# Performance work log

Hardware: AMD Instinct MI355X
Metric: run time of the kernel (lower is better)

The kernel has to match this reference:

```python
import jax, jax.numpy as jnp
import numpy as np

EPS_BN = 1e-5
EPS_NORM = 1e-12
TOP_K = 512


def _conv(x, w):
    # NCHW conv, stride 1, SAME padding (ultralytics Conv autopad)
    return jax.lax.conv_general_dilated(x, w, (1, 1), 'SAME',
                                        dimension_numbers=('NCHW', 'OIHW', 'NCHW'))


def _bn(x, g, b, m, v):
    # inference-mode BatchNorm2d
    inv = jax.lax.rsqrt(v + EPS_BN)
    return (x - m[None, :, None, None]) * (g * inv)[None, :, None, None] + b[None, :, None, None]


def _descriptor(feat, p):
    (w_dr, g_dr, b_dr, m_dr, v_dr,
     w_d1, g_d1, b_d1, m_d1, v_d1,
     g_e, b_e, m_e, v_e,
     w_d2, g_d2, b_d2, m_d2, v_d2) = p
    # dim_reduce: Conv(channel, channel//2, 1) = conv+BN+SiLU
    x = jax.nn.silu(_bn(_conv(feat, w_dr), g_dr, b_dr, m_dr, v_dr))
    # descriptor: Conv(c/2, c/2, 3) + BN + ReLU + Conv(c/2, c/4, 1)
    x = jax.nn.silu(_bn(_conv(x, w_d1), g_d1, b_d1, m_d1, v_d1))
    x = jax.nn.relu(_bn(x, g_e, b_e, m_e, v_e))
    x = jax.nn.silu(_bn(_conv(x, w_d2), g_d2, b_d2, m_d2, v_d2))
    return x


def _keypoints(desc):
    b, c, h, w = desc.shape
    resp = jnp.sqrt(jnp.sum(desc * desc, axis=1)).reshape(b, h * w)  # L2 norm over channels
    _, idx = jax.lax.top_k(resp, TOP_K)                              # [b, K]
    y = (idx // w).astype(desc.dtype) / (h - 1) * 2 - 1
    x = (idx % w).astype(desc.dtype) / (w - 1) * 2 - 1
    return jnp.stack([x, y], axis=-1), idx                           # [b,K,2], [b,K]


def _forward(rgb_feat, ir_feat, params):
    rgb_desc = _descriptor(rgb_feat, params)
    ir_desc = _descriptor(ir_feat, params)

    kp1, idx1 = _keypoints(rgb_desc)
    kp2, idx2 = _keypoints(ir_desc)

    b, c, h, w = rgb_desc.shape
    hw = h * w
    d1 = rgb_desc.reshape(b, c, hw)
    d2 = ir_desc.reshape(b, c, hw)
    d1 = d1 / jnp.maximum(jnp.linalg.norm(d1, axis=1, keepdims=True), EPS_NORM)
    d2 = d2 / jnp.maximum(jnp.linalg.norm(d2, axis=1, keepdims=True), EPS_NORM)
    corr = jnp.einsum('bcn,bcm->bnm', d1, d2)     # [b, hw, hw]
    soft = jax.nn.softmax(corr, axis=-1)

    # scalar matching weight per keypoint pair (gather at keypoint locations)
    bidx = jnp.arange(b)[:, None]
    wts = soft[bidx, idx1, idx2]                  # [b, K]

    # vectorized DLT: A rows, two per point, weighted
    x1, y1 = kp1[..., 0], kp1[..., 1]
    x2, y2 = kp2[..., 0], kp2[..., 1]
    one = jnp.ones_like(x1)
    zer = jnp.zeros_like(x1)
    r1 = jnp.stack([x1, y1, one, zer, zer, zer, -x2 * x1, -x2 * y1, -x2], axis=-1)
    r2 = jnp.stack([zer, zer, zer, x1, y1, one, -y2 * x1, -y2 * y1, -y2], axis=-1)
    A = jnp.stack([r1, r2], axis=2) * wts[:, :, None, None]   # [b,K,2,9]
    A = A.reshape(b, 2 * TOP_K, 9)

    _, _, Vh = jnp.linalg.svd(A, full_matrices=False)          # Vh: [b,9,9]
    # torch.svd returns V; original takes V[-1] == last COLUMN of jax Vh
    H = Vh[:, :, -1].reshape(b, 3, 3)
    return H, rgb_desc, ir_desc


def setup_inputs() -> dict:
    key = jax.random.key(0)
    ks = jax.random.split(key, 8)
    B, C, Hh, Ww = 2, 256, 64, 64
    c2, c4 = C // 2, C // 4
    f32 = jnp.float32

    def bn_params(c):
        return (jnp.ones((c,), f32), jnp.zeros((c,), f32),
                jnp.zeros((c,), f32), jnp.ones((c,), f32))

    g_dr, b_dr, m_dr, v_dr = bn_params(c2)
    g_d1, b_d1, m_d1, v_d1 = bn_params(c2)
    g_e, b_e, m_e, v_e = bn_params(c2)
    g_d2, b_d2, m_d2, v_d2 = bn_params(c4)

    return {
        'rgb_feat': jax.random.normal(ks[0], (B, C, Hh, Ww), f32),
        'ir_feat': jax.random.normal(ks[1], (B, C, Hh, Ww), f32),
        'w_dr': jax.random.normal(ks[2], (c2, C, 1, 1), f32) * 0.05,
        'g_dr': g_dr, 'b_dr': b_dr, 'm_dr': m_dr, 'v_dr': v_dr,
        'w_d1': jax.random.normal(ks[3], (c2, c2, 3, 3), f32) * 0.05,
        'g_d1': g_d1, 'b_d1': b_d1, 'm_d1': m_d1, 'v_d1': v_d1,
        'g_e': g_e, 'b_e': b_e, 'm_e': m_e, 'v_e': v_e,
        'w_d2': jax.random.normal(ks[4], (c4, c2, 1, 1), f32) * 0.05,
        'g_d2': g_d2, 'b_d2': b_d2, 'm_d2': m_d2, 'v_d2': v_d2,
    }


def reference(rgb_feat, ir_feat,
              w_dr, g_dr, b_dr, m_dr, v_dr,
              w_d1, g_d1, b_d1, m_d1, v_d1,
              g_e, b_e, m_e, v_e,
              w_d2, g_d2, b_d2, m_d2, v_d2):
    params = (w_dr, g_dr, b_dr, m_dr, v_dr,
              w_d1, g_d1, b_d1, m_d1, v_d1,
              g_e, b_e, m_e, v_e,
              w_d2, g_d2, b_d2, m_d2, v_d2)
    return _forward(rgb_feat, ir_feat, params)
```

## Files before the change

### kernel.cpp

```cpp
#include <hip/hip_runtime.h>
#include <math.h>


#define HW4 4096
#define NIMG 4

#define OFF_X1   0L
#define OFF_X2   (OFF_X1 + 4L*128*4096)
#define OFF_RESP (OFF_X2 + 4L*128*4096)
#define OFF_INVN (OFF_RESP + 4L*4096)
#define OFF_TOPI (OFF_INVN + 4L*4096)
#define OFF_WTS  (OFF_TOPI + 4L*512)
#define OFF_A    (OFF_WTS + 2L*512)
#define OFF_QN   OFF_X1
#define OFF_PART (OFF_X1 + 65536L)

#define NSPLIT 16

__device__ __forceinline__ float silu_f(float y) { return y / (1.f + expf(-y)); }

__global__ __launch_bounds__(256) void fm_conv1(
    const float* __restrict__ rgb, const float* __restrict__ ir,
    const float* __restrict__ w, const float* __restrict__ g,
    const float* __restrict__ bb, const float* __restrict__ mm,
    const float* __restrict__ vv, float* __restrict__ x1) {
  __shared__ float wl[256*8];
  int bid = blockIdx.x;
  int pblk = bid & 3, ocg = (bid >> 2) & 15, img = bid >> 6;
  int oc0 = ocg * 8;
  int tid = threadIdx.x;
  const float* src = (img < 2) ? (rgb + (long)img*256*HW4) : (ir + (long)(img-2)*256*HW4);
  for (int i = tid; i < 2048; i += 256) {
    int o = i & 7, ic = i >> 3;
    wl[i] = w[(oc0 + o)*256 + ic];
  }
  __syncthreads();
  int p0 = pblk*1024 + tid*4;
  float acc[8][4];
  #pragma unroll
  for (int o = 0; o < 8; ++o)
    #pragma unroll
    for (int j = 0; j < 4; ++j) acc[o][j] = 0.f;
  #pragma unroll 4
  for (int ic = 0; ic < 256; ++ic) {
    float4 v = *(const float4*)(src + (long)ic*HW4 + p0);
    float4 wa = *(const float4*)&wl[ic*8];
    float4 wb = *(const float4*)&wl[ic*8 + 4];
    acc[0][0] = fmaf(wa.x, v.x, acc[0][0]); acc[0][1] = fmaf(wa.x, v.y, acc[0][1]);
    acc[0][2] = fmaf(wa.x, v.z, acc[0][2]); acc[0][3] = fmaf(wa.x, v.w, acc[0][3]);
    acc[1][0] = fmaf(wa.y, v.x, acc[1][0]); acc[1][1] = fmaf(wa.y, v.y, acc[1][1]);
    acc[1][2] = fmaf(wa.y, v.z, acc[1][2]); acc[1][3] = fmaf(wa.y, v.w, acc[1][3]);
    acc[2][0] = fmaf(wa.z, v.x, acc[2][0]); acc[2][1] = fmaf(wa.z, v.y, acc[2][1]);
    acc[2][2] = fmaf(wa.z, v.z, acc[2][2]); acc[2][3] = fmaf(wa.z, v.w, acc[2][3]);
    acc[3][0] = fmaf(wa.w, v.x, acc[3][0]); acc[3][1] = fmaf(wa.w, v.y, acc[3][1]);
    acc[3][2] = fmaf(wa.w, v.z, acc[3][2]); acc[3][3] = fmaf(wa.w, v.w, acc[3][3]);
    acc[4][0] = fmaf(wb.x, v.x, acc[4][0]); acc[4][1] = fmaf(wb.x, v.y, acc[4][1]);
    acc[4][2] = fmaf(wb.x, v.z, acc[4][2]); acc[4][3] = fmaf(wb.x, v.w, acc[4][3]);
    acc[5][0] = fmaf(wb.y, v.x, acc[5][0]); acc[5][1] = fmaf(wb.y, v.y, acc[5][1]);
    acc[5][2] = fmaf(wb.y, v.z, acc[5][2]); acc[5][3] = fmaf(wb.y, v.w, acc[5][3]);
    acc[6][0] = fmaf(wb.z, v.x, acc[6][0]); acc[6][1] = fmaf(wb.z, v.y, acc[6][1]);
    acc[6][2] = fmaf(wb.z, v.z, acc[6][2]); acc[6][3] = fmaf(wb.z, v.w, acc[6][3]);
    acc[7][0] = fmaf(wb.w, v.x, acc[7][0]); acc[7][1] = fmaf(wb.w, v.y, acc[7][1]);
    acc[7][2] = fmaf(wb.w, v.z, acc[7][2]); acc[7][3] = fmaf(wb.w, v.w, acc[7][3]);
  }
  #pragma unroll
  for (int o = 0; o < 8; ++o) {
    int oc = oc0 + o;
    float inv = 1.f / sqrtf(vv[oc] + 1e-5f);
    float sc = g[oc]*inv, sh = bb[oc] - mm[oc]*sc;
    float4 r;
    r.x = silu_f(acc[o][0]*sc + sh);
    r.y = silu_f(acc[o][1]*sc + sh);
    r.z = silu_f(acc[o][2]*sc + sh);
    r.w = silu_f(acc[o][3]*sc + sh);
    r.x = silu_f((acc[o][0] - mm[oc])*sc + bb[oc]);
    r.y = silu_f((acc[o][1] - mm[oc])*sc + bb[oc]);
    r.z = silu_f((acc[o][2] - mm[oc])*sc + bb[oc]);
    r.w = silu_f((acc[o][3] - mm[oc])*sc + bb[oc]);
    *(float4*)(x1 + ((long)img*128 + oc)*HW4 + p0) = r;
  }
}

#define C3_TW 72
#define C3_TR 18
__global__ __launch_bounds__(256) void fm_conv3(
    const float* __restrict__ x1, const float* __restrict__ w,
    const float* __restrict__ g1, const float* __restrict__ b1,
    const float* __restrict__ m1, const float* __restrict__ v1,
    const float* __restrict__ ge, const float* __restrict__ be,
    const float* __restrict__ me, const float* __restrict__ ve,
    float* __restrict__ x2) {
  __shared__ float t[2][4][C3_TR*C3_TW];
  __shared__ float wl[2][4][9][8];
  int bid = blockIdx.x;
  int rt = bid & 3, ocg = (bid >> 2) & 15, img = bid >> 6;
  int oc0 = ocg * 8;
  int y0 = rt * 16;
  int tid = threadIdx.x;
  int ly = tid >> 4;
  int lx = tid & 15;
  int x0 = lx * 4;
  const float* xim = x1 + (long)img*128*HW4;

  int gbase[5][4];
  int lofs[5];
  #pragma unroll
  for (int t5 = 0; t5 < 5; ++t5) {
    int i = tid + 256*t5;
    if (i < 1224) {
      int q = i / 306, r = i - q*306;
      int row = r / 17, seg = r - row*17;
      int gy = y0 + row - 1;
      lofs[t5] = q*(C3_TR*C3_TW) + row*C3_TW + 4 + seg*4;
      #pragma unroll
      for (int e = 0; e < 4; ++e) {
        int x = seg*4 + e - 1;
        gbase[t5][e] = (gy >= 0 && gy < 64 && x >= 0 && x < 64)
                       ? (q*HW4 + gy*64 + x) : -1;
      }
    } else {
      lofs[t5] = -1;
      #pragma unroll
      for (int e = 0; e < 4; ++e) gbase[t5][e] = -1;
    }
  }
  int wg0 = -1, wl0 = 0, wg1 = -1, wl1 = 0;
  {
// ... 283 lines not shown
      part[idx] = m[r];
      part[idx + 1] = s[r];
    }
  }
}

__global__ __launch_bounds__(256) void fm_comb(
    const float* __restrict__ out, const float* __restrict__ invn,
    const int* __restrict__ topidx, const float* __restrict__ qn,
    const float* __restrict__ part, float* __restrict__ wts) {
  int tid = threadIdx.x;
  int kp = blockIdx.x*4 + (tid >> 6);
  int lane = tid & 63;
  int b = kp >> 9, k = kp & 511;
  int col = topidx[(2 + b)*512 + k];
  const float* d2 = out + 18 + (long)(2 + b)*262144;
  float dot = qn[(long)kp*64 + lane] * d2[lane*HW4 + col];
  #pragma unroll
  for (int off = 1; off < 64; off <<= 1) dot += __shfl_xor(dot, off);
  if (lane == 0) {
    const float* pp = part + (long)kp*NSPLIT*2;
    float M = -INFINITY;
    #pragma unroll
    for (int i = 0; i < NSPLIT; ++i) M = fmaxf(M, pp[2*i]);
    float S = 0.f;
    #pragma unroll
    for (int i = 0; i < NSPLIT; ++i) S += pp[2*i + 1]*expf(pp[2*i] - M);
    float v = dot * invn[(long)(2 + b)*HW4 + col];
    wts[b*512 + k] = expf(v - M)/S;
  }
}

__global__ __launch_bounds__(256) void fm_build(
    const int* __restrict__ topidx, const float* __restrict__ wts,
    float* __restrict__ A) {
  int t = blockIdx.x*256 + threadIdx.x;
  if (t >= 1024) return;
  int b = t >> 9, k = t & 511;
  int i1 = topidx[b*512 + k], i2 = topidx[(2 + b)*512 + k];
  float w = wts[b*512 + k];
  float x1 = (float)(i1 & 63) / 63.f * 2.f - 1.f;
  float y1 = (float)(i1 >> 6) / 63.f * 2.f - 1.f;
  float x2 = (float)(i2 & 63) / 63.f * 2.f - 1.f;
  float y2 = (float)(i2 >> 6) / 63.f * 2.f - 1.f;
  float* r = A + ((long)b*1024 + 2*k)*9;
  r[0] = x1*w;  r[1] = y1*w;  r[2] = w;
  r[3] = 0.f;   r[4] = 0.f;   r[5] = 0.f;
  r[6] = (-x2*x1)*w; r[7] = (-x2*y1)*w; r[8] = (-x2)*w;
  r[9]  = 0.f;  r[10] = 0.f;  r[11] = 0.f;
  r[12] = x1*w; r[13] = y1*w; r[14] = w;
  r[15] = (-y2*x1)*w; r[16] = (-y2*y1)*w; r[17] = (-y2)*w;
}

__device__ void lap_slartg(float f, float g, float* cs, float* sn, float* r) {
  if (g == 0.f) { *cs = 1.f; *sn = 0.f; *r = f; }
  else if (f == 0.f) { *cs = 0.f; *sn = copysignf(1.f, g); *r = fabsf(g); }
  else {
    float d = sqrtf(f*f + g*g);
    *cs = fabsf(f) / d;
    *r = copysignf(d, f);
    *sn = g / (*r);
  }
}

__device__ void lap_slas2(float f, float g, float h, float* ssmin, float* ssmax) {
  float fa = fabsf(f), ga = fabsf(g), ha = fabsf(h);
  float fhmn = fminf(fa, ha), fhmx = fmaxf(fa, ha);
  if (fhmn == 0.f) {
    *ssmin = 0.f;
    if (fhmx == 0.f) *ssmax = ga;
    else {
      float mx = fmaxf(fhmx, ga), mn = fminf(fhmx, ga);
      float q = mn / mx;
      *ssmax = mx * sqrtf(1.f + q*q);
    }
  } else {
    if (ga < fhmx) {
      float as_ = 1.f + fhmn/fhmx;
      float at_ = (fhmx - fhmn)/fhmx;
      float au = ga/fhmx; au = au*au;
      float c = 2.f / (sqrtf(as_*as_ + au) + sqrtf(at_*at_ + au));
      *ssmin = fhmn*c;
      *ssmax = fhmx/c;
    } else {
      float au = fhmx/ga;
      if (au == 0.f) { *ssmin = (fhmn*fhmx)/ga; *ssmax = ga; }
      else {
        float as_ = 1.f + fhmn/fhmx;
        float at_ = (fhmx - fhmn)/fhmx;
        float t1 = as_*au, t2 = at_*au;
        float c = 1.f / (sqrtf(1.f + t1*t1) + sqrtf(1.f + t2*t2));
        float smn = (fhmn*c)*au;
        *ssmin = smn + smn;
        *ssmax = ga/(c + c);
      }
    }
  }
}

__device__ void lap_slasv2(float f, float g, float h, float* ssmin, float* ssmax,
                           float* snr, float* csr, float* snl, float* csl) {
  const float epsv = 5.9604645e-08f;
  float ft = f, fa = fabsf(f), ht = h, ha = fabsf(h);
  int pmax = 1;
  bool swap_ = (ha > fa);
  if (swap_) { pmax = 3; float tmp = ft; ft = ht; ht = tmp; tmp = fa; fa = ha; ha = tmp; }
  float gt = g, ga = fabsf(gt);
  float clt = 0.f, crt = 0.f, slt = 0.f, srt = 0.f;
  if (ga == 0.f) { *ssmin = ha; *ssmax = fa; clt = 1.f; crt = 1.f; slt = 0.f; srt = 0.f; }
  else {
    bool gasmal = true;
    if (ga > fa) {
      pmax = 2;
      if ((fa/ga) < epsv) {
        gasmal = false;
        *ssmax = ga;
        if (ha > 1.f) *ssmin = fa/(ga/ha); else *ssmin = (fa/ga)*ha;
        clt = 1.f; slt = ht/gt; srt = 1.f; crt = ft/gt;
      }
    }
    if (gasmal) {
      float d = fa - ha, l;
      if (d == fa) l = 1.f; else l = d/fa;
      float m_ = gt/ft;
      float t = 2.f - l;
      float mm2 = m_*m_, tt = t*t;
      float s = sqrtf(tt + mm2);
      float r_ = (l == 0.f) ? fabsf(m_) : sqrtf(l*l + mm2);
      float a = 0.5f*(s + r_);
      *ssmin = ha/a;
      *ssmax = fa*a;
      if (mm2 == 0.f) {
        if (l == 0.f) t = copysignf(2.f, ft)*copysignf(1.f, gt);
        else t = gt/copysignf(d, ft) + m_/t;
      } else {
        t = (m_/(s + t) + m_/(r_ + l))*(1.f + a);
      }
      float l2 = sqrtf(t*t + 4.f);
      crt = 2.f/l2;
      srt = t/l2;
      clt = (crt + srt*m_)/a;
      slt = (ht/ft)*srt/a;
    }
  }
  if (swap_) { *csl = srt; *snl = crt; *csr = slt; *snr = clt; }
  else { *csl = clt; *snl = slt; *csr = crt; *snr = srt; }
  float tsign = 1.f;
  if (pmax == 1) tsign = copysignf(1.f, *csr)*copysignf(1.f, *csl)*copysignf(1.f, f);
  if (pmax == 2) tsign = copysignf(1.f, *snr)*copysignf(1.f, *csl)*copysignf(1.f, g);
  if (pmax == 3) tsign = copysignf(1.f, *snr)*copysignf(1.f, *snl)*copysignf(1.f, h);
  *ssmax = copysignf(*ssmax, tsign);
  *ssmin = copysignf(*ssmin, tsign*copysignf(1.f, f)*copysignf(1.f, h));
}

__device__ void lap_bdsqr9(float* dd, float* ee, float VT[][9]) {
  const float eps_ = 5.9604645e-08f;
  const float unfl_ = 1.17549435e-38f;
  const float tol_ = 10.f*eps_;
  const int n = 9;
  for (int i = 0; i < 9; ++i) for (int j = 0; j < 9; ++j) VT[i][j] = (i == j) ? 1.f : 0.f;
  float sminoa = fabsf(dd[0]);
  if (sminoa != 0.f) {
    float mu = sminoa;
    for (int i = 1; i < n; ++i) {
      mu = fabsf(dd[i])*(mu/(mu + fabsf(ee[i-1])));
      sminoa = fminf(sminoa, mu);
      if (sminoa == 0.f) break;
    }
  }
  sminoa = sminoa / 3.f;
  float thresh = fmaxf(tol_*sminoa, 486.f*unfl_);
  int m = n, iter = 0, oldll = -1, oldm = -1, idir = 0;
  float sminl = 0.f;
  float rc[8], rs[8];
  int guard = 0;
  while (guard++ < 20000) {
    if (m <= 1) break;
    if (iter > 486) break;
    float smax = fabsf(dd[m-1]);
    int ll = 0; bool split = false;
    for (int lll = 1; lll <= m - 1; ++lll) {
      int l2 = m - lll;
      float abss = fabsf(dd[l2-1]);
      float abse = fabsf(ee[l2-1]);
      if (abse <= thresh) { ll = l2; split = true; break; }
      smax = fmaxf(smax, fmaxf(abss, abse));
    }
    if (split) {
      ee[ll-1] = 0.f;
      if (ll == m - 1) { m = m - 1; continue; }
    } else ll = 0;
    ll = ll + 1;
    if (ll == m - 1) {
      float sigmn, sigmx, sinr, cosr, sinl_, cosl_;
      lap_slasv2(dd[m-2], ee[m-2], dd[m-1], &sigmn, &sigmx, &sinr, &cosr, &sinl_, &cosl_);
      dd[m-2] = sigmx; ee[m-2] = 0.f; dd[m-1] = sigmn;
      for (int j = 0; j < 9; ++j) {
        float xt = VT[m-2][j], yt = VT[m-1][j];
        VT[m-2][j] = cosr*xt + sinr*yt;
        VT[m-1][j] = cosr*yt - sinr*xt;
      }
      m -= 2; continue;
    }
    if (ll > oldm || m < oldll) idir = (fabsf(dd[ll-1]) >= fabsf(dd[m-1])) ? 1 : 2;
    bool conv = false;
    if (idir == 1) {
      if (fabsf(ee[m-2]) <= tol_*fabsf(dd[m-1])) { ee[m-2] = 0.f; continue; }
      float mu = fabsf(dd[ll-1]);
      sminl = mu;
      for (int lll = ll; lll <= m - 1; ++lll) {
        if (fabsf(ee[lll-1]) <= tol_*mu) { ee[lll-1] = 0.f; conv = true; break; }
        mu = fabsf(dd[lll])*(mu/(mu + fabsf(ee[lll-1])));
        sminl = fminf(sminl, mu);
      }
    } else {
      if (fabsf(ee[ll-1]) <= tol_*fabsf(dd[ll-1])) { ee[ll-1] = 0.f; continue; }
      float mu = fabsf(dd[m-1]);
      sminl = mu;
      for (int lll = m - 1; lll >= ll; --lll) {
        if (fabsf(ee[lll-1]) <= tol_*mu) { ee[lll-1] = 0.f; conv = true; break; }
        mu = fabsf(dd[lll-1])*(mu/(mu + fabsf(ee[lll-1])));
        sminl = fminf(sminl, mu);
      }
    }
    if (conv) continue;
    oldll = ll; oldm = m;
    float shift = 0.f, rdum;
    if (!((float)n*tol_*(sminl/smax) <= fmaxf(eps_, 0.01f*tol_))) {
      float sll;
      if (idir == 1) { sll = fabsf(dd[ll-1]); lap_slas2(dd[m-2], ee[m-2], dd[m-1], &shift, &rdum); }
      else           { sll = fabsf(dd[m-1]);  lap_slas2(dd[ll-1], ee[ll-1], dd[ll], &shift, &rdum); }
      if (sll > 0.f) { float q = shift/sll; if (q*q < eps_) shift = 0.f; }
    }
    iter += m - ll;
    if (shift == 0.f) {
      if (idir == 1) {
        float cs = 1.f, oldcs = 1.f, sn = 0.f, oldsn = 0.f, r;
        for (int i = ll; i <= m - 1; ++i) {
          lap_slartg(dd[i-1]*cs, ee[i-1], &cs, &sn, &r);
          if (i > ll) ee[i-2] = oldsn*r;
          float dn;
          lap_slartg(oldcs*r, dd[i]*sn, &oldcs, &oldsn, &dn);
          dd[i-1] = dn;
          rc[i-ll] = cs; rs[i-ll] = sn;
        }
        float h2 = dd[m-1]*cs;
        dd[m-1] = h2*oldcs;
        ee[m-2] = h2*oldsn;
        for (int k2 = 0; k2 <= m - ll - 1; ++k2) {
          int r0 = ll + k2 - 1;
          float c = rc[k2], s = rs[k2];
          for (int j = 0; j < 9; ++j) {
            float t = VT[r0+1][j];
            VT[r0+1][j] = c*t - s*VT[r0][j];
            VT[r0][j]   = s*t + c*VT[r0][j];
          }
        }
        if (fabsf(ee[m-2]) <= thresh) ee[m-2] = 0.f;
      } else {
        float cs = 1.f, oldcs = 1.f, sn = 0.f, oldsn = 0.f, r;
        for (int i = m; i >= ll + 1; --i) {
          lap_slartg(dd[i-1]*cs, ee[i-2], &cs, &sn, &r);
          if (i < m) ee[i-1] = oldsn*r;
          float dn;
          lap_slartg(oldcs*r, dd[i-2]*sn, &oldcs, &oldsn, &dn);
          dd[i-1] = dn;
          rc[i-ll-1] = oldcs; rs[i-ll-1] = -oldsn;
        }
        float h2 = dd[ll-1]*cs;
        dd[ll-1] = h2*oldcs;
        ee[ll-1] = h2*oldsn;
        for (int k2 = m - ll - 1; k2 >= 0; --k2) {
          int r0 = ll + k2 - 1;
          float c = rc[k2], s = rs[k2];
          for (int j = 0; j < 9; ++j) {
            float t = VT[r0+1][j];
            VT[r0+1][j] = c*t - s*VT[r0][j];
            VT[r0][j]   = s*t + c*VT[r0][j];
          }
        }
        if (fabsf(ee[ll-1]) <= thresh) ee[ll-1] = 0.f;
      }
    } else {
      if (idir == 1) {
        float f2 = (fabsf(dd[ll-1]) - shift)*(copysignf(1.f, dd[ll-1]) + shift/dd[ll-1]);
        float g2 = ee[ll-1];
        for (int i = ll; i <= m - 1; ++i) {
          float cr, sr, cl, sl, r;
          lap_slartg(f2, g2, &cr, &sr, &r);
          if (i > ll) ee[i-2] = r;
          f2 = cr*dd[i-1] + sr*ee[i-1];
          ee[i-1] = cr*ee[i-1] - sr*dd[i-1];
          g2 = sr*dd[i];
          dd[i] = cr*dd[i];
          lap_slartg(f2, g2, &cl, &sl, &r);
          dd[i-1] = r;
          f2 = cl*ee[i-1] + sl*dd[i];
          dd[i] = cl*dd[i] - sl*ee[i-1];
          if (i < m - 1) { g2 = sl*ee[i]; ee[i] = cl*ee[i]; }
          rc[i-ll] = cr; rs[i-ll] = sr;
        }
        ee[m-2] = f2;
        for (int k2 = 0; k2 <= m - ll - 1; ++k2) {
          int r0 = ll + k2 - 1;
          float c = rc[k2], s = rs[k2];
          for (int j = 0; j < 9; ++j) {
            float t = VT[r0+1][j];
            VT[r0+1][j] = c*t - s*VT[r0][j];
            VT[r0][j]   = s*t + c*VT[r0][j];
          }
        }
        if (fabsf(ee[m-2]) <= thresh) ee[m-2] = 0.f;
      } else {
        float f2 = (fabsf(dd[m-1]) - shift)*(copysignf(1.f, dd[m-1]) + shift/dd[m-1]);
        float g2 = ee[m-2];
        for (int i = m; i >= ll + 1; --i) {
          float cr, sr, cl, sl, r;
          lap_slartg(f2, g2, &cr, &sr, &r);
          if (i < m) ee[i-1] = r;
          f2 = cr*dd[i-1] + sr*ee[i-2];
          ee[i-2] = cr*ee[i-2] - sr*dd[i-1];
          g2 = sr*dd[i-2];
          dd[i-2] = cr*dd[i-2];
          lap_slartg(f2, g2, &cl, &sl, &r);
          dd[i-1] = r;
          f2 = cl*ee[i-2] + sl*dd[i-2];
          dd[i-2] = cl*dd[i-2] - sl*ee[i-2];
          if (i > ll + 1) { g2 = sl*ee[i-3]; ee[i-3] = cl*ee[i-3]; }
          rc[i-ll-1] = cl; rs[i-ll-1] = -sl;
        }
        ee[ll-1] = f2;
        if (fabsf(ee[ll-1]) <= thresh) ee[ll-1] = 0.f;
        for (int k2 = m - ll - 1; k2 >= 0; --k2) {
          int r0 = ll + k2 - 1;
          float c = rc[k2], s = rs[k2];
          for (int j = 0; j < 9; ++j) {
            float t = VT[r0+1][j];
            VT[r0+1][j] = c*t - s*VT[r0][j];
            VT[r0][j]   = s*t + c*VT[r0][j];
          }
        }
      }
    }
  }
  for (int i = 0; i < n; ++i) {
    if (dd[i] < 0.f) {
      dd[i] = -dd[i];
      for (int j = 0; j < 9; ++j) VT[i][j] = -VT[i][j];
    }
  }
  for (int i = 1; i <= n - 1; ++i) {
    int isub = 1; float smin2 = dd[0];
    for (int j = 2; j <= n + 1 - i; ++j)
      if (dd[j-1] <= smin2) { isub = j; smin2 = dd[j-1]; }
    int tgt = n + 1 - i;
    if (isub != tgt) {
      dd[isub-1] = dd[tgt-1]; dd[tgt-1] = smin2;
      for (int j = 0; j < 9; ++j) {
        float t = VT[isub-1][j]; VT[isub-1][j] = VT[tgt-1][j]; VT[tgt-1][j] = t;
      }
    }
  }
}

__global__ __launch_bounds__(256) void fm_svd(
    const float* __restrict__ Aglob, float* __restrict__ outH) {
  __shared__ float As[1024*9];
  __shared__ float red[256];
  __shared__ float bc[4];
  __shared__ float Rm[9][9], VT[9][9], PT[9][9];
  __shared__ float dd[9], ee[9], taup[9];
  int b = blockIdx.x, tid = threadIdx.x;
  const float* Ab = Aglob + (long)b*1024*9;
  for (int i = tid; i < 9216; i += 256) As[i] = Ab[i];
  __syncthreads();
  for (int k = 0; k < 9; ++k) {
    float ps = 0.f;
    for (int r = k + 1 + tid; r < 1024; r += 256) { float x = As[r*9 + k]; ps = fmaf(x, x, ps); }
    red[tid] = ps; __syncthreads();
    for (int off = 128; off > 0; off >>= 1) {
      if (tid < off) red[tid] += red[tid + off];
      __syncthreads();
    }
    if (tid == 0) {
      float ssq = red[0];
      float alpha = As[k*9 + k];
      float tau = 0.f, sc = 0.f, beta = alpha;
      if (ssq != 0.f) {
        beta = -copysignf(sqrtf(alpha*alpha + ssq), alpha);
        tau = (beta - alpha)/beta;
        sc = 1.f/(alpha - beta);
      }
      bc[0] = tau; bc[1] = sc; bc[2] = beta;
    }
    __syncthreads();
    float tau = bc[0], sc = bc[1];
    if (tau != 0.f) {
      for (int r = k + 1 + tid; r < 1024; r += 256) As[r*9 + k] *= sc;
    }
    __syncthreads();
    if (tau != 0.f) {
      for (int j = k + 1; j < 9; ++j) {
        float pd = 0.f;
        for (int r = k + 1 + tid; r < 1024; r += 256) pd = fmaf(As[r*9 + k], As[r*9 + j], pd);
        red[tid] = pd; __syncthreads();
        for (int off = 128; off > 0; off >>= 1) {
          if (tid < off) red[tid] += red[tid + off];
          __syncthreads();
        }
        float s = (red[0] + As[k*9 + j]) * tau;
        if (tid == 0) As[k*9 + j] -= s;
        for (int r = k + 1 + tid; r < 1024; r += 256) As[r*9 + j] -= s*As[r*9 + k];
        __syncthreads();
      }
    }
    if (tid == 0) As[k*9 + k] = bc[2];
    __syncthreads();
  }
  if (tid == 0) {
    for (int i = 0; i < 9; ++i)
      for (int j = 0; j < 9; ++j)
        Rm[i][j] = (j >= i) ? As[i*9 + j] : 0.f;
    for (int i = 0; i < 9; ++i) {
      float alpha = Rm[i][i];
      float ssq = 0.f;
      for (int r = i + 1; r < 9; ++r) ssq += Rm[r][i]*Rm[r][i];
      float tauq = 0.f, beta = alpha;
      if (ssq != 0.f) {
        beta = -copysignf(sqrtf(alpha*alpha + ssq), alpha);
        tauq = (beta - alpha)/beta;
        float sc = 1.f/(alpha - beta);
        for (int r = i + 1; r < 9; ++r) Rm[r][i] *= sc;
      }
      dd[i] = beta;
      if (tauq != 0.f) {
        for (int j = i + 1; j < 9; ++j) {
          float s = Rm[i][j];
          for (int r = i + 1; r < 9; ++r) s += Rm[r][i]*Rm[r][j];
          s *= tauq;
          Rm[i][j] -= s;
          for (int r = i + 1; r < 9; ++r) Rm[r][j] -= s*Rm[r][i];
        }
      }
      if (i < 8) {
        float alpha2 = Rm[i][i+1];
        float ssq2 = 0.f;
        for (int c = i + 2; c < 9; ++c) ssq2 += Rm[i][c]*Rm[i][c];
        float tp = 0.f, beta2 = alpha2;
        if (ssq2 != 0.f) {
          beta2 = -copysignf(sqrtf(alpha2*alpha2 + ssq2), alpha2);
          tp = (beta2 - alpha2)/beta2;
          float sc = 1.f/(alpha2 - beta2);
          for (int c = i + 2; c < 9; ++c) Rm[i][c] *= sc;
        }
        ee[i] = beta2;
        taup[i] = tp;
        if (tp != 0.f) {
          for (int r = i + 1; r < 9; ++r) {
            float s = Rm[r][i+1];
            for (int c = i + 2; c < 9; ++c) s += Rm[i][c]*Rm[r][c];
            s *= tp;
            Rm[r][i+1] -= s;
            for (int c = i + 2; c < 9; ++c) Rm[r][c] -= s*Rm[i][c];
          }
        }
      }
    }
    for (int i = 0; i < 9; ++i) for (int j = 0; j < 9; ++j) PT[i][j] = (i == j) ? 1.f : 0.f;
    for (int i = 0; i < 8; ++i) {
      float tp = taup[i];
      if (tp == 0.f) continue;
      for (int j = 0; j < 9; ++j) {
        float s = PT[i+1][j];
        for (int r = i + 2; r < 9; ++r) s += Rm[i][r]*PT[r][j];
        s *= tp;
        PT[i+1][j] -= s;
        for (int r = i + 2; r < 9; ++r) PT[r][j] -= s*Rm[i][r];
      }
    }
    lap_bdsqr9(dd, ee, VT);
    for (int i = 0; i < 9; ++i) {
      float s = 0.f;
      for (int k2 = 0; k2 < 9; ++k2) s += VT[i][k2]*PT[k2][8];
      outH[b*9 + i] = s;
    }
  }
}

extern "C" void kernel_launch(void* const* d_in, const int* in_sizes, int n_in,
                              void* d_out, int out_size, void* d_ws, size_t ws_size,
                              hipStream_t stream) {
  const float* rgb  = (const float*)d_in[0];
  const float* ir   = (const float*)d_in[1];
  const float* w_dr = (const float*)d_in[2];
  const float* g_dr = (const float*)d_in[3];
  const float* b_dr = (const float*)d_in[4];
  const float* m_dr = (const float*)d_in[5];
  const float* v_dr = (const float*)d_in[6];
  const float* w_d1 = (const float*)d_in[7];
  const float* g_d1 = (const float*)d_in[8];
  const float* b_d1 = (const float*)d_in[9];
  const float* m_d1 = (const float*)d_in[10];
  const float* v_d1 = (const float*)d_in[11];
  const float* g_e  = (const float*)d_in[12];
  const float* b_e  = (const float*)d_in[13];
  const float* m_e  = (const float*)d_in[14];
  const float* v_e  = (const float*)d_in[15];
  const float* w_d2 = (const float*)d_in[16];
  const float* g_d2 = (const float*)d_in[17];
  const float* b_d2 = (const float*)d_in[18];
  const float* m_d2 = (const float*)d_in[19];
  const float* v_d2 = (const float*)d_in[20];

  float* out = (float*)d_out;
  float* ws  = (float*)d_ws;
  float* x1   = ws + OFF_X1;
  float* x2   = ws + OFF_X2;
  float* resp = ws + OFF_RESP;
  float* invn = ws + OFF_INVN;
  int*   topi = (int*)(ws + OFF_TOPI);
  float* wts  = ws + OFF_WTS;
  float* Amat = ws + OFF_A;
  float* qn   = ws + OFF_QN;
  float* part = ws + OFF_PART;

  fm_conv1<<<256, 256, 0, stream>>>(rgb, ir, w_dr, g_dr, b_dr, m_dr, v_dr, x1);
  fm_conv3<<<256, 256, 0, stream>>>(x1, w_d1, g_d1, b_d1, m_d1, v_d1,
                                    g_e, b_e, m_e, v_e, x2);
  fm_conv2<<<256, 256, 0, stream>>>(x2, w_d2, g_d2, b_d2, m_d2, v_d2, out);
  fm_resp<<<(NIMG*HW4 + 255)/256, 256, 0, stream>>>(out, resp, invn);
  fm_sort<<<NIMG, 1024, 0, stream>>>(resp, topi);
  fm_qgather<<<256, 256, 0, stream>>>(out, invn, topi, qn);
  fm_corr<<<dim3(NSPLIT, 16, 2), 256, 0, stream>>>(out, invn, qn, part);
  fm_comb<<<256, 256, 0, stream>>>(out, invn, topi, qn, part, wts);
  fm_build<<<4, 256, 0, stream>>>(topi, wts, Amat);
  fm_svd<<<2, 256, 0, stream>>>(Amat, out);
}
// ... 1 lines not shown
```

Before: 443.5 us.

## Move SVD small-matrix stage into registers with wavefront shuffles and batched reflector updates

Restructures the fm_svd kernel. The Householder QR of the 1024x9 system now replaces 256-thread LDS tree reductions with wave shuffle reductions, and batches all column dot products per reflector so one reduction and sync pass covers them. The 9x9 bidiagonalization and bdsqr iterations now run in registers: each of the first 9 lanes tracks one column of VT instead of a single thread rotating a shared 9x9 matrix. Only column 8 of PT is built. Fully unrolled predicated loops add register pressure and extra instructions. The iteration guard is also reduced, and a dead BN epilogue duplicate is removed from conv1.

```diff
diff --git a/kernel.cpp b/kernel.cpp
--- a/kernel.cpp
+++ b/kernel.cpp
@@ -67,12 +67,8 @@
   for (int o = 0; o < 8; ++o) {
     int oc = oc0 + o;
     float inv = 1.f / sqrtf(vv[oc] + 1e-5f);
-    float sc = g[oc]*inv, sh = bb[oc] - mm[oc]*sc;
+    float sc = g[oc]*inv;
     float4 r;
-    r.x = silu_f(acc[o][0]*sc + sh);
-    r.y = silu_f(acc[o][1]*sc + sh);
-    r.z = silu_f(acc[o][2]*sc + sh);
-    r.w = silu_f(acc[o][3]*sc + sh);
     r.x = silu_f((acc[o][0] - mm[oc])*sc + bb[oc]);
     r.y = silu_f((acc[o][1] - mm[oc])*sc + bb[oc]);
     r.z = silu_f((acc[o][2] - mm[oc])*sc + bb[oc]);
@@ -462,7 +458,7 @@
   r[15] = (-y2*x1)*w; r[16] = (-y2*y1)*w; r[17] = (-y2)*w;
 }
 
-__device__ void lap_slartg(float f, float g, float* cs, float* sn, float* r) {
+__device__ __forceinline__ void lap_slartg(float f, float g, float* cs, float* sn, float* r) {
   if (g == 0.f) { *cs = 1.f; *sn = 0.f; *r = f; }
   else if (f == 0.f) { *cs = 0.f; *sn = copysignf(1.f, g); *r = fabsf(g); }
   else {
@@ -473,7 +469,7 @@
   }
 }
 
-__device__ void lap_slas2(float f, float g, float h, float* ssmin, float* ssmax) {
+__device__ __forceinline__ void lap_slas2(float f, float g, float h, float* ssmin, float* ssmax) {
   float fa = fabsf(f), ga = fabsf(g), ha = fabsf(h);
   float fhmn = fminf(fa, ha), fhmx = fmaxf(fa, ha);
   if (fhmn == 0.f) {
@@ -508,7 +504,7 @@
   }
 }
 
-__device__ void lap_slasv2(float f, float g, float h, float* ssmin, float* ssmax,
+__device__ __forceinline__ void lap_slasv2(float f, float g, float h, float* ssmin, float* ssmax,
                            float* snr, float* csr, float* snl, float* csl) {
   const float epsv = 5.9604645e-08f;
   float ft = f, fa = fabsf(f), ht = h, ha = fabsf(h);
@@ -563,212 +559,220 @@
   *ssmin = copysignf(*ssmin, tsign*copysignf(1.f, f)*copysignf(1.f, h));
 }
 
-__device__ void lap_bdsqr9(float* dd, float* ee, float VT[][9]) {
+__device__ __forceinline__ float get9(const float (&a)[9], int idx) {
+  float v = a[0];
+#pragma unroll
+  for (int i = 1; i < 9; ++i) if (idx == i) v = a[i];
+  return v;
+}
+__device__ __forceinline__ void set9(float (&a)[9], int idx, float val) {
+#pragma unroll
+  for (int i = 0; i < 9; ++i) if (idx == i) a[i] = val;
+}
+
+__device__ __forceinline__ void bdsqr9_reg(float (&dd)[9], float (&ee)[9], float (&vt)[9]) {
   const float eps_ = 5.9604645e-08f;
   const float unfl_ = 1.17549435e-38f;
   const float tol_ = 10.f*eps_;
-  const int n = 9;
-  for (int i = 0; i < 9; ++i) for (int j = 0; j < 9; ++j) VT[i][j] = (i == j) ? 1.f : 0.f;
   float sminoa = fabsf(dd[0]);
   if (sminoa != 0.f) {
     float mu = sminoa;
-    for (int i = 1; i < n; ++i) {
-      mu = fabsf(dd[i])*(mu/(mu + fabsf(ee[i-1])));
-      sminoa = fminf(sminoa, mu);
-      if (sminoa == 0.f) break;
+    bool z = false;
+#pragma unroll
+    for (int i = 1; i < 9; ++i) {
+      if (!z) {
+        mu = fabsf(dd[i])*(mu/(mu + fabsf(ee[i-1])));
+        sminoa = fminf(sminoa, mu);
+        if (sminoa == 0.f) z = true;
+      }
     }
   }
   sminoa = sminoa / 3.f;
   float thresh = fmaxf(tol_*sminoa, 486.f*unfl_);
-  int m = n, iter = 0, oldll = -1, oldm = -1, idir = 0;
+  int m = 9, iter = 0, oldll = -1, oldm = -1, idir = 0;
   float sminl = 0.f;
-  float rc[8], rs[8];
   int guard = 0;
-  while (guard++ < 20000) {
+  while (guard++ < 2000) {
     if (m <= 1) break;
     if (iter > 486) break;
-    float smax = fabsf(dd[m-1]);
+    float smax = fabsf(get9(dd, m-1));
     int ll = 0; bool split = false;
-    for (int lll = 1; lll <= m - 1; ++lll) {
-      int l2 = m - lll;
-      float abss = fabsf(dd[l2-1]);
-      float abse = fabsf(ee[l2-1]);
-      if (abse <= thresh) { ll = l2; split = true; break; }
-      smax = fmaxf(smax, fmaxf(abss, abse));
+#pragma unroll
+    for (int l2 = 8; l2 >= 1; --l2) {
+      if (l2 <= m - 1 && !split) {
+        float abss = fabsf(dd[l2-1]);
+        float abse = fabsf(ee[l2-1]);
+        if (abse <= thresh) { ll = l2; split = true; }
+        else smax = fmaxf(smax, fmaxf(abss, abse));
+      }
     }
     if (split) {
-      ee[ll-1] = 0.f;
+      set9(ee, ll-1, 0.f);
       if (ll == m - 1) { m = m - 1; continue; }
     } else ll = 0;
     ll = ll + 1;
     if (ll == m - 1) {
+      float d1 = get9(dd, m-2), e1 = get9(ee, m-2), d2v = get9(dd, m-1);
       float sigmn, sigmx, sinr, cosr, sinl_, cosl_;
-      lap_slasv2(dd[m-2], ee[m-2], dd[m-1], &sigmn, &sigmx, &sinr, &cosr, &sinl_, &cosl_);
-      dd[m-2] = sigmx; ee[m-2] = 0.f; dd[m-1] = sigmn;
-      for (int j = 0; j < 9; ++j) {
-        float xt = VT[m-2][j], yt = VT[m-1][j];
-        VT[m-2][j] = cosr*xt + sinr*yt;
-        VT[m-1][j] = cosr*yt - sinr*xt;
-      }
+      lap_slasv2(d1, e1, d2v, &sigmn, &sigmx, &sinr, &cosr, &sinl_, &cosl_);
+      set9(dd, m-2, sigmx); set9(ee, m-2, 0.f); set9(dd, m-1, sigmn);
+      float xt = get9(vt, m-2), yt = get9(vt, m-1);
+      set9(vt, m-2, cosr*xt + sinr*yt);
+      set9(vt, m-1, cosr*yt - sinr*xt);
       m -= 2; continue;
     }
-    if (ll > oldm || m < oldll) idir = (fabsf(dd[ll-1]) >= fabsf(dd[m-1])) ? 1 : 2;
+    if (ll > oldm || m < oldll)
+      idir = (fabsf(get9(dd, ll-1)) >= fabsf(get9(dd, m-1))) ? 1 : 2;
     bool conv = false;
     if (idir == 1) {
-      if (fabsf(ee[m-2]) <= tol_*fabsf(dd[m-1])) { ee[m-2] = 0.f; continue; }
-      float mu = fabsf(dd[ll-1]);
+      if (fabsf(get9(ee, m-2)) <= tol_*fabsf(get9(dd, m-1))) { set9(ee, m-2, 0.f); continue; }
+      float mu = fabsf(get9(dd, ll-1));
       sminl = mu;
-      for (int lll = ll; lll <= m - 1; ++lll) {
-        if (fabsf(ee[lll-1]) <= tol_*mu) { ee[lll-1] = 0.f; conv = true; break; }
-        mu = fabsf(dd[lll])*(mu/(mu + fabsf(ee[lll-1])));
-        sminl = fminf(sminl, mu);
+#pragma unroll
+      for (int lll = 1; lll <= 8; ++lll) {
+        if (lll >= ll && lll <= m - 1 && !conv) {
+          if (fabsf(ee[lll-1]) <= tol_*mu) { ee[lll-1] = 0.f; conv = true; }
+          else {
+            mu = fabsf(dd[lll])*(mu/(mu + fabsf(ee[lll-1])));
+            sminl = fminf(sminl, mu);
+          }
+        }
       }
     } else {
-      if (fabsf(ee[ll-1]) <= tol_*fabsf(dd[ll-1])) { ee[ll-1] = 0.f; continue; }
-      float mu = fabsf(dd[m-1]);
+      if (fabsf(get9(ee, ll-1)) <= tol_*fabsf(get9(dd, ll-1))) { set9(ee, ll-1, 0.f); continue; }
+      float mu = fabsf(get9(dd, m-1));
       sminl = mu;
-      for (int lll = m - 1; lll >= ll; --lll) {
-        if (fabsf(ee[lll-1]) <= tol_*mu) { ee[lll-1] = 0.f; conv = true; break; }
-        mu = fabsf(dd[lll-1])*(mu/(mu + fabsf(ee[lll-1])));
-        sminl = fminf(sminl, mu);
+#pragma unroll
+      for (int lll = 8; lll >= 1; --lll) {
+        if (lll <= m - 1 && lll >= ll && !conv) {
+          if (fabsf(ee[lll-1]) <= tol_*mu) { ee[lll-1] = 0.f; conv = true; }
+          else {
+            mu = fabsf(dd[lll-1])*(mu/(mu + fabsf(ee[lll-1])));
+            sminl = fminf(sminl, mu);
+          }
+        }
       }
     }
     if (conv) continue;
     oldll = ll; oldm = m;
     float shift = 0.f, rdum;
-    if (!((float)n*tol_*(sminl/smax) <= fmaxf(eps_, 0.01f*tol_))) {
+    if (!(9.f*tol_*(sminl/smax) <= fmaxf(eps_, 0.01f*tol_))) {
       float sll;
-      if (idir == 1) { sll = fabsf(dd[ll-1]); lap_slas2(dd[m-2], ee[m-2], dd[m-1], &shift, &rdum); }
-      else           { sll = fabsf(dd[m-1]);  lap_slas2(dd[ll-1], ee[ll-1], dd[ll], &shift, &rdum); }
+      if (idir == 1) { sll = fabsf(get9(dd, ll-1)); lap_slas2(get9(dd, m-2), get9(ee, m-2), get9(dd, m-1), &shift, &rdum); }
+      else           { sll = fabsf(get9(dd, m-1));  lap_slas2(get9(dd, ll-1), get9(ee, ll-1), get9(dd, ll), &shift, &rdum); }
       if (sll > 0.f) { float q = shift/sll; if (q*q < eps_) shift = 0.f; }
     }
     iter += m - ll;
     if (shift == 0.f) {
       if (idir == 1) {
         float cs = 1.f, oldcs = 1.f, sn = 0.f, oldsn = 0.f, r;
-        for (int i = ll; i <= m - 1; ++i) {
-          lap_slartg(dd[i-1]*cs, ee[i-1], &cs, &sn, &r);
-          if (i > ll) ee[i-2] = oldsn*r;
-          float dn;
-          lap_slartg(oldcs*r, dd[i]*sn, &oldcs, &oldsn, &dn);
-          dd[i-1] = dn;
-          rc[i-ll] = cs; rs[i-ll] = sn;
-        }
-        float h2 = dd[m-1]*cs;
-        dd[m-1] = h2*oldcs;
-        ee[m-2] = h2*oldsn;
-        for (int k2 = 0; k2 <= m - ll - 1; ++k2) {
-          int r0 = ll + k2 - 1;
-          float c = rc[k2], s = rs[k2];
-          for (int j = 0; j < 9; ++j) {
-            float t = VT[r0+1][j];
-            VT[r0+1][j] = c*t - s*VT[r0][j];
-            VT[r0][j]   = s*t + c*VT[r0][j];
+#pragma unroll
+        for (int i = 1; i <= 8; ++i) {
+          if (i >= ll && i <= m - 1) {
+            lap_slartg(dd[i-1]*cs, ee[i-1], &cs, &sn, &r);
+            if (i >= 2 && i > ll) ee[i-2] = oldsn*r;
+            float dn;
+            lap_slartg(oldcs*r, dd[i]*sn, &oldcs, &oldsn, &dn);
+            dd[i-1] = dn;
+            float t = vt[i]; vt[i] = cs*t - sn*vt[i-1]; vt[i-1] = sn*t + cs*vt[i-1];
           }
         }
-        if (fabsf(ee[m-2]) <= thresh) ee[m-2] = 0.f;
+        float h2 = get9(dd, m-1)*cs;
+        set9(dd, m-1, h2*oldcs);
+        set9(ee, m-2, h2*oldsn);
+        if (fabsf(get9(ee, m-2)) <= thresh) set9(ee, m-2, 0.f);
       } else {
         float cs = 1.f, oldcs = 1.f, sn = 0.f, oldsn = 0.f, r;
-        for (int i = m; i >= ll + 1; --i) {
-          lap_slartg(dd[i-1]*cs, ee[i-2], &cs, &sn, &r);
-          if (i < m) ee[i-1] = oldsn*r;
-          float dn;
-          lap_slartg(oldcs*r, dd[i-2]*sn, &oldcs, &oldsn, &dn);
-          dd[i-1] = dn;
-          rc[i-ll-1] = oldcs; rs[i-ll-1] = -oldsn;
-        }
-        float h2 = dd[ll-1]*cs;
-        dd[ll-1] = h2*oldcs;
-        ee[ll-1] = h2*oldsn;
-        for (int k2 = m - ll - 1; k2 >= 0; --k2) {
-          int r0 = ll + k2 - 1;
-          float c = rc[k2], s = rs[k2];
-          for (int j = 0; j < 9; ++j) {
-            float t = VT[r0+1][j];
-            VT[r0+1][j] = c*t - s*VT[r0][j];
-            VT[r0][j]   = s*t + c*VT[r0][j];
+#pragma unroll
+        for (int i = 9; i >= 2; --i) {
+          if (i <= m && i >= ll + 1) {
+            lap_slartg(dd[i-1]*cs, ee[i-2], &cs, &sn, &r);
+            if (i < m) ee[i-1] = oldsn*r;
+            float dn;
+            lap_slartg(oldcs*r, dd[i-2]*sn, &oldcs, &oldsn, &dn);
+            dd[i-1] = dn;
+            float c2 = oldcs, s2 = -oldsn;
+            float t = vt[i-1]; vt[i-1] = c2*t - s2*vt[i-2]; vt[i-2] = s2*t + c2*vt[i-2];
           }
         }
-        if (fabsf(ee[ll-1]) <= thresh) ee[ll-1] = 0.f;
+        float h2 = get9(dd, ll-1)*cs;
+        set9(dd, ll-1, h2*oldcs);
+        set9(ee, ll-1, h2*oldsn);
+        if (fabsf(get9(ee, ll-1)) <= thresh) set9(ee, ll-1, 0.f);
       }
     } else {
       if (idir == 1) {
-        float f2 = (fabsf(dd[ll-1]) - shift)*(copysignf(1.f, dd[ll-1]) + shift/dd[ll-1]);
-        float g2 = ee[ll-1];
-        for (int i = ll; i <= m - 1; ++i) {
-          float cr, sr, cl, sl, r;
-          lap_slartg(f2, g2, &cr, &sr, &r);
-          if (i > ll) ee[i-2] = r;
-          f2 = cr*dd[i-1] + sr*ee[i-1];
-          ee[i-1] = cr*ee[i-1] - sr*dd[i-1];
-          g2 = sr*dd[i];
-          dd[i] = cr*dd[i];
-          lap_slartg(f2, g2, &cl, &sl, &r);
-          dd[i-1] = r;
-          f2 = cl*ee[i-1] + sl*dd[i];
-          dd[i] = cl*dd[i] - sl*ee[i-1];
-          if (i < m - 1) { g2 = sl*ee[i]; ee[i] = cl*ee[i]; }
-          rc[i-ll] = cr; rs[i-ll] = sr;
-        }
-        ee[m-2] = f2;
-        for (int k2 = 0; k2 <= m - ll - 1; ++k2) {
-          int r0 = ll + k2 - 1;
-          float c = rc[k2], s = rs[k2];
-          for (int j = 0; j < 9; ++j) {
-            float t = VT[r0+1][j];
-            VT[r0+1][j] = c*t - s*VT[r0][j];
-            VT[r0][j]   = s*t + c*VT[r0][j];
+        float d0 = get9(dd, ll-1);
+        float f2 = (fabsf(d0) - shift)*(copysignf(1.f, d0) + shift/d0);
+        float g2 = get9(ee, ll-1);
+#pragma unroll
+        for (int i = 1; i <= 8; ++i) {
+          if (i >= ll && i <= m - 1) {
+            float cr, sr, cl, sl, r;
+            lap_slartg(f2, g2, &cr, &sr, &r);
+            if (i >= 2 && i > ll) ee[i-2] = r;
+            f2 = cr*dd[i-1] + sr*ee[i-1];
+            ee[i-1] = cr*ee[i-1] - sr*dd[i-1];
+            g2 = sr*dd[i];
+            dd[i] = cr*dd[i];
+            lap_slartg(f2, g2, &cl, &sl, &r);
+            dd[i-1] = r;
+            f2 = cl*ee[i-1] + sl*dd[i];
+            dd[i] = cl*dd[i] - sl*ee[i-1];
+            if (i < m - 1) { g2 = sl*ee[i]; ee[i] = cl*ee[i]; }
+            float t = vt[i]; vt[i] = cr*t - sr*vt[i-1]; vt[i-1] = sr*t + cr*vt[i-1];
           }
         }
-        if (fabsf(ee[m-2]) <= thresh) ee[m-2] = 0.f;
+        set9(ee, m-2, f2);
+        if (fabsf(get9(ee, m-2)) <= thresh) set9(ee, m-2, 0.f);
       } else {
-        float f2 = (fabsf(dd[m-1]) - shift)*(copysignf(1.f, dd[m-1]) + shift/dd[m-1]);
-        float g2 = ee[m-2];
-        for (int i = m; i >= ll + 1; --i) {
-          float cr, sr, cl, sl, r;
-          lap_slartg(f2, g2, &cr, &sr, &r);
-          if (i < m) ee[i-1] = r;
-          f2 = cr*dd[i-1] + sr*ee[i-2];
-          ee[i-2] = cr*ee[i-2] - sr*dd[i-1];
-          g2 = sr*dd[i-2];
-          dd[i-2] = cr*dd[i-2];
-          lap_slartg(f2, g2, &cl, &sl, &r);
-          dd[i-1] = r;
-          f2 = cl*ee[i-2] + sl*dd[i-2];
-          dd[i-2] = cl*dd[i-2] - sl*ee[i-2];
-          if (i > ll + 1) { g2 = sl*ee[i-3]; ee[i-3] = cl*ee[i-3]; }
-          rc[i-ll-1] = cl; rs[i-ll-1] = -sl;
-        }
-        ee[ll-1] = f2;
-        if (fabsf(ee[ll-1]) <= thresh) ee[ll-1] = 0.f;
-        for (int k2 = m - ll - 1; k2 >= 0; --k2) {
-          int r0 = ll + k2 - 1;
-          float c = rc[k2], s = rs[k2];
-          for (int j = 0; j < 9; ++j) {
-            float t = VT[r0+1][j];
-            VT[r0+1][j] = c*t - s*VT[r0][j];
-            VT[r0][j]   = s*t + c*VT[r0][j];
+        float dm = get9(dd, m-1);
+        float f2 = (fabsf(dm) - shift)*(copysignf(1.f, dm) + shift/dm);
+        float g2 = get9(ee, m-2);
+#pragma unroll
+        for (int i = 9; i >= 2; --i) {
+          if (i <= m && i >= ll + 1) {
+            float cr, sr, cl, sl, r;
+            lap_slartg(f2, g2, &cr, &sr, &r);
+            if (i < m) ee[i-1] = r;
+            f2 = cr*dd[i-1] + sr*ee[i-2];
+            ee[i-2] = cr*ee[i-2] - sr*dd[i-1];
+            g2 = sr*dd[i-2];
+            dd[i-2] = cr*dd[i-2];
+            lap_slartg(f2, g2, &cl, &sl, &r);
+            dd[i-1] = r;
+            f2 = cl*ee[i-2] + sl*dd[i-2];
+            dd[i-2] = cl*dd[i-2] - sl*ee[i-2];
+            if (i >= 3 && i > ll + 1) { g2 = sl*ee[i-3]; ee[i-3] = cl*ee[i-3]; }
+            float c2 = cl, s2 = -sl;
+            float t = vt[i-1]; vt[i-1] = c2*t - s2*vt[i-2]; vt[i-2] = s2*t + c2*vt[i-2];
           }
         }
-      }
-    }
-  }
-  for (int i = 0; i < n; ++i) {
-    if (dd[i] < 0.f) {
-      dd[i] = -dd[i];
-      for (int j = 0; j < 9; ++j) VT[i][j] = -VT[i][j];
-    }
-  }
-  for (int i = 1; i <= n - 1; ++i) {
+        set9(ee, ll-1, f2);
+        if (fabsf(get9(ee, ll-1)) <= thresh) set9(ee, ll-1, 0.f);
+      }
+    }
+  }
+#pragma unroll
+  for (int i = 0; i < 9; ++i) {
+    if (dd[i] < 0.f) { dd[i] = -dd[i]; vt[i] = -vt[i]; }
+  }
+#pragma unroll
+  for (int i = 1; i <= 8; ++i) {
     int isub = 1; float smin2 = dd[0];
-    for (int j = 2; j <= n + 1 - i; ++j)
-      if (dd[j-1] <= smin2) { isub = j; smin2 = dd[j-1]; }
-    int tgt = n + 1 - i;
+#pragma unroll
+    for (int j = 2; j <= 9; ++j) {
+      if (j <= 10 - i) {
+        if (dd[j-1] <= smin2) { isub = j; smin2 = dd[j-1]; }
+      }
+    }
+    const int tgt = 10 - i;
     if (isub != tgt) {
-      dd[isub-1] = dd[tgt-1]; dd[tgt-1] = smin2;
-      for (int j = 0; j < 9; ++j) {
-        float t = VT[isub-1][j]; VT[isub-1][j] = VT[tgt-1][j]; VT[tgt-1][j] = t;
-      }
+      set9(dd, isub-1, dd[tgt-1]);
+      dd[tgt-1] = smin2;
+      float tv = get9(vt, isub-1);
+      set9(vt, isub-1, vt[tgt-1]);
+      vt[tgt-1] = tv;
     }
   }
 }
@@ -776,24 +780,29 @@
 __global__ __launch_bounds__(256) void fm_svd(
     const float* __restrict__ Aglob, float* __restrict__ outH) {
   __shared__ float As[1024*9];
-  __shared__ float red[256];
+  __shared__ float wred[4][12];
   __shared__ float bc[4];
-  __shared__ float Rm[9][9], VT[9][9], PT[9][9];
-  __shared__ float dd[9], ee[9], taup[9];
   int b = blockIdx.x, tid = threadIdx.x;
-  const float* Ab = Aglob + (long)b*1024*9;
-  for (int i = tid; i < 9216; i += 256) As[i] = Ab[i];
+  int wv = tid >> 6, ln = tid & 63;
+  const float* Ab = Aglob + (long)b*9216;
+  {
+    const float4* s4 = (const float4*)Ab;
+    float4* d4 = (float4*)As;
+#pragma unroll
+    for (int t = 0; t < 9; ++t) d4[tid + 256*t] = s4[tid + 256*t];
+  }
   __syncthreads();
   for (int k = 0; k < 9; ++k) {
     float ps = 0.f;
-    for (int r = k + 1 + tid; r < 1024; r += 256) { float x = As[r*9 + k]; ps = fmaf(x, x, ps); }
-    red[tid] = ps; __syncthreads();
-    for (int off = 128; off > 0; off >>= 1) {
-      if (tid < off) red[tid] += red[tid + off];
-      __syncthreads();
-    }
+    for (int r = k + 1 + tid; r < 1024; r += 256) {
+      float x = As[r*9 + k]; ps = fmaf(x, x, ps);
+    }
+#pragma unroll
+    for (int off = 1; off < 64; off <<= 1) ps += __shfl_xor(ps, off);
+    if (ln == 0) wred[wv][8] = ps;
+    __syncthreads();
     if (tid == 0) {
-      float ssq = red[0];
+      float ssq = wred[0][8] + wred[1][8] + wred[2][8] + wred[3][8];
       float alpha = As[k*9 + k];
       float tau = 0.f, sc = 0.f, beta = alpha;
       if (ssq != 0.f) {
@@ -810,89 +819,152 @@
     }
     __syncthreads();
     if (tau != 0.f) {
-      for (int j = k + 1; j < 9; ++j) {
-        float pd = 0.f;
-        for (int r = k + 1 + tid; r < 1024; r += 256) pd = fmaf(As[r*9 + k], As[r*9 + j], pd);
-        red[tid] = pd; __syncthreads();
-        for (int off = 128; off > 0; off >>= 1) {
-          if (tid < off) red[tid] += red[tid + off];
-          __syncthreads();
-        }
-        float s = (red[0] + As[k*9 + j]) * tau;
-        if (tid == 0) As[k*9 + j] -= s;
-        for (int r = k + 1 + tid; r < 1024; r += 256) As[r*9 + j] -= s*As[r*9 + k];
-        __syncthreads();
+      float pd[8];
+#pragma unroll
+      for (int jj = 0; jj < 8; ++jj) pd[jj] = 0.f;
+      for (int r = k + 1 + tid; r < 1024; r += 256) {
+        float vk = As[r*9 + k];
+#pragma unroll
+        for (int jj = 0; jj < 8; ++jj) {
+          int j = k + 1 + jj;
+          if (j < 9) pd[jj] = fmaf(vk, As[r*9 + j], pd[jj]);
+        }
+      }
+#pragma unroll
+      for (int off = 1; off < 64; off <<= 1) {
+#pragma unroll
+        for (int jj = 0; jj < 8; ++jj) pd[jj] += __shfl_xor(pd[jj], off);
+      }
+      if (ln == 0) {
+#pragma unroll
+        for (int jj = 0; jj < 8; ++jj) wred[wv][jj] = pd[jj];
+      }
+      __syncthreads();
+      float sj[8];
+#pragma unroll
+      for (int jj = 0; jj < 8; ++jj) {
+        int j = k + 1 + jj;
+        float v = 0.f;
+        if (j < 9)
+          v = (wred[0][jj] + wred[1][jj] + wred[2][jj] + wred[3][jj] + As[k*9 + j]) * tau;
+        sj[jj] = v;
+      }
+      for (int r = k + 1 + tid; r < 1024; r += 256) {
+        float vk = As[r*9 + k];
+#pragma unroll
+        for (int jj = 0; jj < 8; ++jj) {
+          int j = k + 1 + jj;
+          if (j < 9) As[r*9 + j] -= sj[jj]*vk;
+        }
+      }
+      __syncthreads();
+      if (tid == 0) {
+#pragma unroll
+        for (int jj = 0; jj < 8; ++jj) {
+          int j = k + 1 + jj;
+          if (j < 9) As[k*9 + j] -= sj[jj];
+        }
       }
     }
     if (tid == 0) As[k*9 + k] = bc[2];
     __syncthreads();
   }
-  if (tid == 0) {
+  if (tid < 64) {
+    float R[9][9];
+#pragma unroll
     for (int i = 0; i < 9; ++i)
+#pragma unroll
       for (int j = 0; j < 9; ++j)
-        Rm[i][j] = (j >= i) ? As[i*9 + j] : 0.f;
+        R[i][j] = (j >= i) ? As[i*9 + j] : 0.f;
+    float dd[9], ee[9], taupv[8], pt8[9];
+    ee[8] = 0.f;
+#pragma unroll
     for (int i = 0; i < 9; ++i) {
-      float alpha = Rm[i][i];
+      float alpha = R[i][i];
       float ssq = 0.f;
-      for (int r = i + 1; r < 9; ++r) ssq += Rm[r][i]*Rm[r][i];
+#pragma unroll
+      for (int r2 = i + 1; r2 < 9; ++r2) ssq += R[r2][i]*R[r2][i];
       float tauq = 0.f, beta = alpha;
       if (ssq != 0.f) {
         beta = -copysignf(sqrtf(alpha*alpha + ssq), alpha);
         tauq = (beta - alpha)/beta;
-        float sc = 1.f/(alpha - beta);
-        for (int r = i + 1; r < 9; ++r) Rm[r][i] *= sc;
+        float scq = 1.f/(alpha - beta);
+#pragma unroll
+        for (int r2 = i + 1; r2 < 9; ++r2) R[r2][i] *= scq;
       }
       dd[i] = beta;
       if (tauq != 0.f) {
+#pragma unroll
         for (int j = i + 1; j < 9; ++j) {
-          float s = Rm[i][j];
-          for (int r = i + 1; r < 9; ++r) s += Rm[r][i]*Rm[r][j];
+          float s = R[i][j];
+#pragma unroll
+          for (int r2 = i + 1; r2 < 9; ++r2) s += R[r2][i]*R[r2][j];
           s *= tauq;
-          Rm[i][j] -= s;
-          for (int r = i + 1; r < 9; ++r) Rm[r][j] -= s*Rm[r][i];
+          R[i][j] -= s;
+#pragma unroll
+          for (int r2 = i + 1; r2 < 9; ++r2) R[r2][j] -= s*R[r2][i];
         }
       }
       if (i < 8) {
-        float alpha2 = Rm[i][i+1];
+        float alpha2 = R[i][i+1];
         float ssq2 = 0.f;
-        for (int c = i + 2; c < 9; ++c) ssq2 += Rm[i][c]*Rm[i][c];
+#pragma unroll
+        for (int c = i + 2; c < 9; ++c) ssq2 += R[i][c]*R[i][c];
         float tp = 0.f, beta2 = alpha2;
         if (ssq2 != 0.f) {
           beta2 = -copysignf(sqrtf(alpha2*alpha2 + ssq2), alpha2);
           tp = (beta2 - alpha2)/beta2;
-          float sc = 1.f/(alpha2 - beta2);
-          for (int c = i + 2; c < 9; ++c) Rm[i][c] *= sc;
+          float scp = 1.f/(alpha2 - beta2);
+#pragma unroll
+          for (int c = i + 2; c < 9; ++c) R[i][c] *= scp;
         }
         ee[i] = beta2;
-        taup[i] = tp;
+        taupv[i] = tp;
         if (tp != 0.f) {
-          for (int r = i + 1; r < 9; ++r) {
-            float s = Rm[r][i+1];
-            for (int c = i + 2; c < 9; ++c) s += Rm[i][c]*Rm[r][c];
+#pragma unroll
+          for (int r2 = i + 1; r2 < 9; ++r2) {
+            float s = R[r2][i+1];
+#pragma unroll
+            for (int c = i + 2; c < 9; ++c) s += R[i][c]*R[r2][c];
             s *= tp;
-            Rm[r][i+1] -= s;
-            for (int c = i + 2; c < 9; ++c) Rm[r][c] -= s*Rm[i][c];
+            R[r2][i+1] -= s;
+#pragma unroll
+            for (int c = i + 2; c < 9; ++c) R[r2][c] -= s*R[i][c];
           }
         }
       }
     }
-    for (int i = 0; i < 9; ++i) for (int j = 0; j < 9; ++j) PT[i][j] = (i == j) ? 1.f : 0.f;
+#pragma unroll
+    for (int i = 0; i < 9; ++i) pt8[i] = (i == 8) ? 1.f : 0.f;
+#pragma unroll
     for (int i = 0; i < 8; ++i) {
-      float tp = taup[i];
-      if (tp == 0.f) continue;
-      for (int j = 0; j < 9; ++j) {
-        float s = PT[i+1][j];
-        for (int r = i + 2; r < 9; ++r) s += Rm[i][r]*PT[r][j];
+      float tp = taupv[i];
+      if (tp != 0.f) {
+        float s = pt8[i+1];
+#pragma unroll
+        for (int r2 = i + 2; r2 < 9; ++r2) s += R[i][r2]*pt8[r2];
         s *= tp;
-        PT[i+1][j] -= s;
-        for (int r = i + 2; r < 9; ++r) PT[r][j] -= s*Rm[i][r];
-      }
-    }
-    lap_bdsqr9(dd, ee, VT);
-    for (int i = 0; i < 9; ++i) {
-      float s = 0.f;
-      for (int k2 = 0; k2 < 9; ++k2) s += VT[i][k2]*PT[k2][8];
-      outH[b*9 + i] = s;
+        pt8[i+1] -= s;
+#pragma unroll
+        for (int r2 = i + 2; r2 < 9; ++r2) pt8[r2] -= s*R[i][r2];
+      }
+    }
+    float vt[9];
+#pragma unroll
+    for (int i = 0; i < 9; ++i) vt[i] = (i == tid) ? 1.f : 0.f;
+    bdsqr9_reg(dd, ee, vt);
+    float p8 = (tid < 9) ? get9(pt8, tid) : 0.f;
+    float h[9];
+#pragma unroll
+    for (int i = 0; i < 9; ++i) h[i] = vt[i]*p8;
+#pragma unroll
+    for (int off = 1; off < 16; off <<= 1) {
+#pragma unroll
+      for (int i = 0; i < 9; ++i) h[i] += __shfl_xor(h[i], off);
+    }
+    if (tid == 0) {
+#pragma unroll
+      for (int i = 0; i < 9; ++i) outH[b*9 + i] = h[i];
     }
   }
 }
```

After: 385.3 us (median of 3 runs). 13.1% less time.
